# Optimization experiments

Hardware: AMD Instinct MI355X
Metric: run time of the kernel (lower is better)

Reference implementation:

```python
import jax, jax.numpy as jnp
import numpy as np

N_TP = 4  # number of heterogeneous agent types (experts)


def _mlp(x, w1, b1, w2, b2, w3, b3):
    h = jax.nn.relu(x @ w1 + b1)
    h = jax.nn.relu(h @ w2 + b2)
    return h @ w3 + b3


def setup_inputs() -> dict:
    key = jax.random.key(0)
    ks = jax.random.split(key, 12)
    T, A, D, H, NA = 2048, 128, 64, 64, 16
    s = 0.05
    return {
        "obs": jax.random.normal(ks[0], (T, A, D), dtype=jnp.float32),
        "hete_pick": jax.random.randint(ks[1], (T, A), 0, N_TP, dtype=jnp.int64),
        "gp_sel_summary": jax.random.uniform(ks[2], (T, N_TP), dtype=jnp.float32),
        "W1": jax.random.normal(ks[3], (N_TP, D + N_TP, H), dtype=jnp.float32) * s,
        "b1": jnp.zeros((N_TP, H), jnp.float32),
        "W2": jax.random.normal(ks[4], (N_TP, H, H), dtype=jnp.float32) * s,
        "b2": jnp.zeros((N_TP, H), jnp.float32),
        "W3": jax.random.normal(ks[5], (N_TP, H, NA), dtype=jnp.float32) * s,
        "b3": jnp.zeros((N_TP, NA), jnp.float32),
        "cW1": jax.random.normal(ks[6], (D + N_TP, H), dtype=jnp.float32) * s,
        "cb1": jnp.zeros((H,), jnp.float32),
        "cW2": jax.random.normal(ks[7], (H, H), dtype=jnp.float32) * s,
        "cb2": jnp.zeros((H,), jnp.float32),
        "cW3": jax.random.normal(ks[8], (H, 1), dtype=jnp.float32) * s,
        "cb3": jnp.zeros((1,), jnp.float32),
    }


def reference(obs, hete_pick, gp_sel_summary, W1, b1, W2, b2, W3, b3,
              cW1, cb1, cW2, cb2, cW3, cb3):
    T, A, D = obs.shape
    n_tp = W1.shape[0]
    # hete_info_obs: broadcast group-selection summary over agents, concat to obs
    hete_info = jnp.broadcast_to(gp_sel_summary[:, None, :], (T, A, n_tp))
    x = jnp.concatenate([obs, hete_info.astype(obs.dtype)], axis=-1)  # [T,A,D+n_tp]
    xf = x.reshape(T * A, D + n_tp)
    tp = hete_pick.reshape(T * A)
    # per-type dispatch: mask -> sub-net -> scatter back (expressed as masked select)
    logits = jnp.zeros((T * A, W3.shape[-1]), obs.dtype)
    for t in range(n_tp):
        out_t = _mlp(xf, W1[t], b1[t], W2[t], b2[t], W3[t], b3[t])
        logits = jnp.where((tp == t)[:, None], out_t, logits)
    # central critic runs on all agents
    value = _mlp(xf, cW1, cb1, cW2, cb2, cW3, cb3)  # [T*A,1]
    out = jnp.concatenate([logits, value], axis=-1)  # [T*A, n_action+1]
    return out.reshape(T, A, -1)
```

## Files before the change

kernel.cpp:

```cpp
#include <hip/hip_runtime.h>
#include <stdint.h>


typedef float v4f __attribute__((ext_vector_type(4)));
typedef short v8s __attribute__((ext_vector_type(8)));
typedef short v4s __attribute__((ext_vector_type(4)));
typedef float v4fa __attribute__((ext_vector_type(4), aligned(4)));

#define XS_STR 72
#define HS_STR 136
#define WP2_OFF  30720
#define WP3_OFF  51200
#define WPB2_OFF 56320

#define SEL4(te, a0, a1, a2, a3) \
    ((te) < 2 ? ((te) == 0 ? (a0) : (a1)) : ((te) == 2 ? (a2) : (a3)))

static __device__ __forceinline__ short f2bf(float f) {
    union { __bf16 b; short s; } u;
    u.b = (__bf16)f;
    return u.s;
}

static __device__ __forceinline__ v4s pack4r(const v4f a) {
    v4s r;
    r[0] = f2bf(fmaxf(a[0], 0.f));
    r[1] = f2bf(fmaxf(a[1], 0.f));
    r[2] = f2bf(fmaxf(a[2], 0.f));
    r[3] = f2bf(fmaxf(a[3], 0.f));
    return r;
}

__global__ void prep_kernel(const float* __restrict__ W1, const float* __restrict__ cW1,
                            const float* __restrict__ W2, const float* __restrict__ cW2,
                            const float* __restrict__ W3, const float* __restrict__ cW3,
                            const float* __restrict__ b1, const float* __restrict__ cb1,
                            const float* __restrict__ b2, const float* __restrict__ cb2,
                            short* __restrict__ wp) {
    int b = blockIdx.x, lane = threadIdx.x;
    int nl = lane & 15, quad = lane >> 4;
    short frag[8];
    if (b < 60) {
        int e = b / 12, rem = b % 12, ks = rem / 4, nt = rem % 4;
        int n = nt * 16 + nl;
#pragma unroll
        for (int j = 0; j < 8; j++) {
            int k = ks * 32 + quad * 8 + j;
            float v = 0.f;
            if (k < 68)       v = (e < 4) ? W1[(e * 68 + k) * 64 + n] : cW1[k * 64 + n];
            else if (k == 68) v = (e < 4) ? b1[e * 64 + n] : cb1[n];
            frag[j] = f2bf(v);
        }
    } else if (b < 100) {
        int u = b - 60, e = u / 8, ks = (u % 8) / 4, nt = u % 4;
        int n = nt * 16 + nl;
#pragma unroll
        for (int j = 0; j < 8; j++) {
            int k = ks * 32 + quad * 8 + j;
            frag[j] = f2bf((e < 4) ? W2[(e * 64 + k) * 64 + n] : cW2[k * 64 + n]);
        }
    } else if (b < 110) {
        int u = b - 100;
#pragma unroll
        for (int j = 0; j < 8; j++) {
            int ks = (u < 8) ? (u & 1) : (u - 8);
            int k  = ks * 32 + quad * 8 + j;
            float v;
            if (u < 8) { int ee = u >> 1; v = W3[(ee * 64 + k) * 16 + nl]; }
            else       { v = (nl == 0) ? cW3[k] : 0.f; }
            frag[j] = f2bf(v);
        }
    } else {
        int u = b - 110, net = u / 4, nt = u % 4;
        int n = nt * 16 + nl;
#pragma unroll
        for (int j = 0; j < 8; j++) {
            float v = 0.f;
            if (quad == 0 && j == 0) v = (net < 4) ? b2[net * 64 + n] : cb2[n];
            frag[j] = f2bf(v);
        }
    }
    v8s pk = { frag[0], frag[1], frag[2], frag[3], frag[4], frag[5], frag[6], frag[7] };
    *(v8s*)(wp + (size_t)b * 512 + lane * 8) = pk;
}


__global__ __launch_bounds__(256, 4) void main_kernel(
    const float* __restrict__ obs, const int* __restrict__ hete,
    const float* __restrict__ gp, const short* __restrict__ wp,
    const float* __restrict__ b3, const float* __restrict__ cb3,
    float* __restrict__ out)
{
    __shared__ __align__(16) short buf[128 * HS_STR];
    __shared__ int rowtok[128];
    __shared__ int tslot[128];
    __shared__ int wcnt[2][4];

    short* xs = buf;
    short* hs = buf;

    const int b = blockIdx.x;
    const int tid = threadIdx.x, lane = tid & 63, w = tid >> 6;
    const int ml = lane & 15, quad = lane >> 4;
    const size_t base = (size_t)b * 128;

    const int ltk = tid >> 1, hh = tid & 1;
    const float4* src = (const float4*)(obs + (base + ltk) * 64 + hh * 32);
    float4 f[8];
#pragma unroll
    for (int t = 0; t < 8; t++) f[t] = src[t];

    const float* gpb = gp + (size_t)b * 4;
    float g0 = gpb[0], g1 = gpb[1], g2 = gpb[2], g3 = gpb[3];

    int e = 0, rank = 0;
    if (tid < 128) {
        e = hete[base + tid];
        unsigned long long ltm = (1ull << lane) - 1ull;
        unsigned long long m0 = __ballot(e == 0);
        unsigned long long m1 = __ballot(e == 1);
        unsigned long long m2 = __ballot(e == 2);
        unsigned long long m3 = __ballot(e == 3);
        if      (e == 0) rank = __popcll(m0 & ltm);
        else if (e == 1) rank = __popcll(m1 & ltm);
        else if (e == 2) rank = __popcll(m2 & ltm);
        else             rank = __popcll(m3 & ltm);
        if (lane == 0) {
            wcnt[w][0] = __popcll(m0); wcnt[w][1] = __popcll(m1);
            wcnt[w][2] = __popcll(m2); wcnt[w][3] = __popcll(m3);
        }
    }
    __syncthreads();

    const int c0 = wcnt[0][0] + wcnt[1][0];
    const int c1 = wcnt[0][1] + wcnt[1][1];
    const int c2 = wcnt[0][2] + wcnt[1][2];
    const int sgs1 = __builtin_amdgcn_readfirstlane(c0);
    const int sgs2 = __builtin_amdgcn_readfirstlane(c0 + c1);
    const int sgs3 = __builtin_amdgcn_readfirstlane(c0 + c1 + c2);
    const int SG[5] = { 0, sgs1, sgs2, sgs3, 128 };

    if (tid < 128) {
        int gsE  = SEL4(e, 0, sgs1, sgs2, sgs3);
        int woff = (w == 1) ? wcnt[0][e] : 0;
        int slot = gsE + woff + rank;
        rowtok[slot] = tid;
        tslot[tid]   = slot;
    }
    __syncthreads();

    {
        int s  = tslot[ltk];
        int rb = s * XS_STR + hh * 32;
#pragma unroll
        for (int t = 0; t < 4; t++) {
            float4 a0 = f[2 * t], a1 = f[2 * t + 1];
            v8s pk = { f2bf(a0.x), f2bf(a0.y), f2bf(a0.z), f2bf(a0.w),
                       f2bf(a1.x), f2bf(a1.y), f2bf(a1.z), f2bf(a1.w) };
            *(v8s*)&xs[rb + t * 8] = pk;
        }
    }

    v8s gfrag = (v8s){0,0,0,0,0,0,0,0};
    v8s onef  = (v8s){0,0,0,0,0,0,0,0};
    if (quad == 0) {
        gfrag[0] = f2bf(g0); gfrag[1] = f2bf(g1);
        gfrag[2] = f2bf(g2); gfrag[3] = f2bf(g3);
        gfrag[4] = (short)0x3F80;
        onef[0]  = (short)0x3F80;
    }
    __syncthreads();

    v4f accE[8], accC[8], fx[3];
#pragma unroll
    for (int mt = 0; mt < 8; mt++) { accE[mt] = (v4f){0,0,0,0}; }
    fx[0] = fx[1] = fx[2] = (v4f){0,0,0,0};

    {
        v8s cW2 = *(const v8s*)(wp + (size_t)(14 * 4 + w) * 512 + lane * 8);
        v4f tC = __builtin_amdgcn_mfma_f32_16x16x32_bf16(cW2, gfrag, (v4f){0,0,0,0}, 0, 0, 0);
#pragma unroll
        for (int mt = 0; mt < 8; mt++) accC[mt] = tC;
    }
#pragma unroll
    for (int te = 0; te < 4; te++) {
        int lo = SG[te], hi = SG[te + 1];
        if (lo < hi) {
            v8s aW2 = *(const v8s*)(wp + (size_t)((te * 3 + 2) * 4 + w) * 512 + lane * 8);
            v4f tE = __builtin_amdgcn_mfma_f32_16x16x32_bf16(aW2, gfrag, (v4f){0,0,0,0}, 0, 0, 0);
#pragma unroll
            for (int mt = 0; mt < 8; mt++)
                if (mt * 16 >= lo && mt * 16 < hi) accE[mt] = tE;
            if (te > 0 && (lo & 15)) fx[te - 1] = tE;
        }
    }

    v8s cf1[2];
#pragma unroll
    for (int ks = 0; ks < 2; ks++)
        cf1[ks] = *(const v8s*)(wp + (size_t)((12 + ks) * 4 + w) * 512 + lane * 8);

#pragma unroll
    for (int ks = 0; ks < 2; ks++) {
#pragma unroll
        for (int mt = 0; mt < 8; mt++) {
            v8s xb = *(const v8s*)&xs[(mt * 16 + ml) * XS_STR + ks * 32 + quad * 8];
            accC[mt] = __builtin_amdgcn_mfma_f32_16x16x32_bf16(cf1[ks], xb, accC[mt], 0, 0, 0);
        }
#pragma unroll
        for (int te = 0; te < 4; te++) {
            int lo = SG[te], hi = SG[te + 1];
            if (lo < hi) {
                v8s aW = *(const v8s*)(wp + (size_t)((te * 3 + ks) * 4 + w) * 512 + lane * 8);
#pragma unroll
                for (int mt = 0; mt < 8; mt++) {
                    if (mt * 16 >= lo && mt * 16 < hi) {
                        v8s xb = *(const v8s*)&xs[(mt * 16 + ml) * XS_STR + ks * 32 + quad * 8];
                        accE[mt] = __builtin_amdgcn_mfma_f32_16x16x32_bf16(aW, xb, accE[mt], 0, 0, 0);
                    }
                    if (te > 0 && (lo & 15) && (lo >> 4) == mt) {
                        v8s xb = *(const v8s*)&xs[(mt * 16 + ml) * XS_STR + ks * 32 + quad * 8];
                        fx[te - 1] = __builtin_amdgcn_mfma_f32_16x16x32_bf16(aW, xb, fx[te - 1], 0, 0, 0);
                    }
                }
            }
        }
    }
    __syncthreads();

    {
#pragma unroll
        for (int mt = 0; mt < 8; mt++) {
            int rb = (mt * 16 + ml) * HS_STR + w * 16 + quad * 4;
            *(v4s*)&hs[rb]      = pack4r(accE[mt]);
            *(v4s*)&hs[rb + 64] = pack4r(accC[mt]);
        }
#pragma unroll
        for (int bb = 0; bb < 3; bb++) {
            int lo = SG[bb + 1], hi = SG[bb + 2];
            if ((lo & 15) && lo < hi) {
                int row  = (lo >> 4) * 16 + ml;
                int erow = (row >= sgs1) + (row >= sgs2) + (row >= sgs3);
                if (erow == bb + 1)
                    *(v4s*)&hs[row * HS_STR + w * 16 + quad * 4] = pack4r(fx[bb]);
            }
        }
    }
    __syncthreads();

    v4f acc2E[8], acc2C[8], fx2[3];
#pragma unroll
    for (int mt = 0; mt < 8; mt++) { acc2E[mt] = (v4f){0,0,0,0}; }
    fx2[0] = fx2[1] = fx2[2] = (v4f){0,0,0,0};

    {
        v8s cbf = *(const v8s*)(wp + WPB2_OFF + (size_t)(16 + w) * 512 + lane * 8);
        v4f tC = __builtin_amdgcn_mfma_f32_16x16x32_bf16(cbf, onef, (v4f){0,0,0,0}, 0, 0, 0);
#pragma unroll
        for (int mt = 0; mt < 8; mt++) acc2C[mt] = tC;
    }
#pragma unroll
    for (int te = 0; te < 4; te++) {
        int lo = SG[te], hi = SG[te + 1];
        if (lo < hi) {
            v8s bf = *(const v8s*)(wp + WPB2_OFF + (size_t)(te * 4 + w) * 512 + lane * 8);
            v4f tE = __builtin_amdgcn_mfma_f32_16x16x32_bf16(bf, onef, (v4f){0,0,0,0}, 0, 0, 0);
#pragma unroll
            for (int mt = 0; mt < 8; mt++)
                if (mt * 16 >= lo && mt * 16 < hi) acc2E[mt] = tE;
            if (te > 0 && (lo & 15)) fx2[te - 1] = tE;
        }
    }

    v8s cf2[2];
#pragma unroll
    for (int ks = 0; ks < 2; ks++)
        cf2[ks] = *(const v8s*)(wp + WP2_OFF + (size_t)((8 + ks) * 4 + w) * 512 + lane * 8);

#pragma unroll
    for (int ks = 0; ks < 2; ks++) {
#pragma unroll
        for (int mt = 0; mt < 8; mt++) {
            v8s hC = *(const v8s*)&hs[(mt * 16 + ml) * HS_STR + 64 + ks * 32 + quad * 8];
            acc2C[mt] = __builtin_amdgcn_mfma_f32_16x16x32_bf16(cf2[ks], hC, acc2C[mt], 0, 0, 0);
        }
#pragma unroll
        for (int te = 0; te < 4; te++) {
            int lo = SG[te], hi = SG[te + 1];
            if (lo < hi) {
                v8s aW = *(const v8s*)(wp + WP2_OFF + (size_t)((te * 2 + ks) * 4 + w) * 512 + lane * 8);
#pragma unroll
                for (int mt = 0; mt < 8; mt++) {
                    if (mt * 16 >= lo && mt * 16 < hi) {
                        v8s hE = *(const v8s*)&hs[(mt * 16 + ml) * HS_STR + ks * 32 + quad * 8];
                        acc2E[mt] = __builtin_amdgcn_mfma_f32_16x16x32_bf16(aW, hE, acc2E[mt], 0, 0, 0);
                    }
                    if (te > 0 && (lo & 15) && (lo >> 4) == mt) {
                        v8s hE = *(const v8s*)&hs[(mt * 16 + ml) * HS_STR + ks * 32 + quad * 8];
                        fx2[te - 1] = __builtin_amdgcn_mfma_f32_16x16x32_bf16(aW, hE, fx2[te - 1], 0, 0, 0);
                    }
                }
            }
        }
    }
    __syncthreads();

    {
#pragma unroll
        for (int mt = 0; mt < 8; mt++) {
            int rb = (mt * 16 + ml) * HS_STR + w * 16 + quad * 4;
            *(v4s*)&hs[rb]      = pack4r(acc2E[mt]);
            *(v4s*)&hs[rb + 64] = pack4r(acc2C[mt]);
        }
#pragma unroll
        for (int bb = 0; bb < 3; bb++) {
            int lo = SG[bb + 1], hi = SG[bb + 2];
            if ((lo & 15) && lo < hi) {
                int row  = (lo >> 4) * 16 + ml;
                int erow = (row >= sgs1) + (row >= sgs2) + (row >= sgs3);
                if (erow == bb + 1)
                    *(v4s*)&hs[row * HS_STR + w * 16 + quad * 4] = pack4r(fx2[bb]);
            }
        }
    }
    __syncthreads();

    v4f accL[2], accV[2];
#pragma unroll
    for (int j = 0; j < 2; j++) { accL[j] = (v4f){0,0,0,0}; accV[j] = (v4f){0,0,0,0}; }

#pragma unroll
    for (int ks = 0; ks < 2; ks++) {
        v8s aV = *(const v8s*)(wp + WP3_OFF + (size_t)(8 + ks) * 512 + lane * 8);
#pragma unroll
        for (int j = 0; j < 2; j++) {
            int mt = w + 4 * j;
            int te = (mt * 16 >= sgs1) + (mt * 16 >= sgs2) + (mt * 16 >= sgs3);
            v8s aW = *(const v8s*)(wp + WP3_OFF + (size_t)(te * 2 + ks) * 512 + lane * 8);
            v8s hE = *(const v8s*)&hs[(mt * 16 + ml) * HS_STR + ks * 32 + quad * 8];
            v8s hC = *(const v8s*)&hs[(mt * 16 + ml) * HS_STR + 64 + ks * 32 + quad * 8];
            accL[j] = __builtin_amdgcn_mfma_f32_16x16x32_bf16(aW, hE, accL[j], 0, 0, 0);
            accV[j] = __builtin_amdgcn_mfma_f32_16x16x32_bf16(aV, hC, accV[j], 0, 0, 0);
        }
    }

    v4f fxL[3];
#pragma unroll
    for (int bb = 0; bb < 3; bb++) {
        fxL[bb] = (v4f){0,0,0,0};
        int lo = SG[bb + 1], hi = SG[bb + 2];
        int mtb = lo >> 4;
        if ((lo & 15) && lo < hi && (mtb & 3) == w) {
#pragma unroll
            for (int ks = 0; ks < 2; ks++) {
                v8s aW = *(const v8s*)(wp + WP3_OFF + (size_t)((bb + 1) * 2 + ks) * 512 + lane * 8);
                v8s hE = *(const v8s*)&hs[(mtb * 16 + ml) * HS_STR + ks * 32 + quad * 8];
                fxL[bb] = __builtin_amdgcn_mfma_f32_16x16x32_bf16(aW, hE, fxL[bb], 0, 0, 0);
            }
        }
    }

    {
        float cb3v = cb3[0];
#pragma unroll
        for (int j = 0; j < 2; j++) {
            int mt = w + 4 * j;
            int te = (mt * 16 >= sgs1) + (mt * 16 >= sgs2) + (mt * 16 >= sgs3);
            int row = mt * 16 + ml;
            int erow = (row >= sgs1) + (row >= sgs2) + (row >= sgs3);
            int tk = rowtok[row];
            float* o = out + (base + (size_t)tk) * 17;
            if (erow == te) {
                v4fa b3v = *(const v4fa*)(b3 + te * 16 + quad * 4);
                v4fa ov = { accL[j][0] + b3v[0], accL[j][1] + b3v[1],
                            accL[j][2] + b3v[2], accL[j][3] + b3v[3] };
                *(v4fa*)(o + quad * 4) = ov;
            }
            if (quad == 0) o[16] = accV[j][0] + cb3v;
        }
#pragma unroll
        for (int bb = 0; bb < 3; bb++) {
            int lo = SG[bb + 1], hi = SG[bb + 2];
            int mtb = lo >> 4;
            if ((lo & 15) && lo < hi && (mtb & 3) == w) {
                int row = mtb * 16 + ml;
                int erow = (row >= sgs1) + (row >= sgs2) + (row >= sgs3);
                if (erow == bb + 1) {
                    v4fa b3v = *(const v4fa*)(b3 + (bb + 1) * 16 + quad * 4);
                    int tk = rowtok[row];
                    float* o = out + (base + (size_t)tk) * 17;
                    v4fa ov = { fxL[bb][0] + b3v[0], fxL[bb][1] + b3v[1],
                                fxL[bb][2] + b3v[2], fxL[bb][3] + b3v[3] };
                    *(v4fa*)(o + quad * 4) = ov;
                }
            }
        }
    }
}


extern "C" void kernel_launch(void* const* d_in, const int* in_sizes, int n_in,
                              void* d_out, int out_size, void* d_ws, size_t ws_size,
                              hipStream_t stream) {
    const float* obs = (const float*)d_in[0];
    const int*  hete = (const int*)d_in[1];
    const float* gp  = (const float*)d_in[2];
    const float* W1  = (const float*)d_in[3];
    const float* b1  = (const float*)d_in[4];
    const float* W2  = (const float*)d_in[5];
    const float* b2  = (const float*)d_in[6];
    const float* W3  = (const float*)d_in[7];
    const float* b3  = (const float*)d_in[8];
    const float* cW1 = (const float*)d_in[9];
    const float* cb1 = (const float*)d_in[10];
    const float* cW2 = (const float*)d_in[11];
    const float* cb2 = (const float*)d_in[12];
    const float* cW3 = (const float*)d_in[13];
    const float* cb3 = (const float*)d_in[14];
    float* out = (float*)d_out;

    short* wp = (short*)d_ws;

    prep_kernel<<<130,  64, 0, stream>>>(W1, cW1, W2, cW2, W3, cW3,
                                         b1, cb1, b2, cb2, wp);
    main_kernel<<<2048, 256, 0, stream>>>(obs, hete, gp, wp, b3, cb3, out);
}
```

Baseline: 159.4 us.

## Process two timesteps per block and prefetch next timestep's inputs during compute

Each block now handles two consecutive timesteps in a loop, halving the grid, and issues the global loads for the second timestep's obs, type ids and summary while the first timestep's layer-2 work runs. Tokens are no longer physically permuted into sorted slots in LDS; layer-1 reads gather rows through a per-lane rowtok index, which removes the tslot array. The goal is to hide global load latency and amortize per-block setup. The cost is higher register pressure from the prefetch buffers, which could lower occupancy, and fewer blocks to fill the GPU.

```diff
diff --git a/kernel.cpp b/kernel.cpp
--- a/kernel.cpp
+++ b/kernel.cpp
@@ -12,6 +12,7 @@
 #define WP2_OFF  30720
 #define WP3_OFF  51200
 #define WPB2_OFF 56320
+#define NT 2
 
 #define SEL4(te, a0, a1, a2, a3) \
     ((te) < 2 ? ((te) == 0 ? (a0) : (a1)) : ((te) == 2 ? (a2) : (a3)))
@@ -93,307 +94,330 @@
 {
     __shared__ __align__(16) short buf[128 * HS_STR];
     __shared__ int rowtok[128];
-    __shared__ int tslot[128];
     __shared__ int wcnt[2][4];
 
     short* xs = buf;
     short* hs = buf;
 
-    const int b = blockIdx.x;
     const int tid = threadIdx.x, lane = tid & 63, w = tid >> 6;
     const int ml = lane & 15, quad = lane >> 4;
-    const size_t base = (size_t)b * 128;
-
+    const int ts0 = blockIdx.x * NT;
     const int ltk = tid >> 1, hh = tid & 1;
-    const float4* src = (const float4*)(obs + (base + ltk) * 64 + hh * 32);
+
     float4 f[8];
-#pragma unroll
-    for (int t = 0; t < 8; t++) f[t] = src[t];
-
-    const float* gpb = gp + (size_t)b * 4;
-    float g0 = gpb[0], g1 = gpb[1], g2 = gpb[2], g3 = gpb[3];
-
-    int e = 0, rank = 0;
-    if (tid < 128) {
-        e = hete[base + tid];
-        unsigned long long ltm = (1ull << lane) - 1ull;
-        unsigned long long m0 = __ballot(e == 0);
-        unsigned long long m1 = __ballot(e == 1);
-        unsigned long long m2 = __ballot(e == 2);
-        unsigned long long m3 = __ballot(e == 3);
-        if      (e == 0) rank = __popcll(m0 & ltm);
-        else if (e == 1) rank = __popcll(m1 & ltm);
-        else if (e == 2) rank = __popcll(m2 & ltm);
-        else             rank = __popcll(m3 & ltm);
-        if (lane == 0) {
-            wcnt[w][0] = __popcll(m0); wcnt[w][1] = __popcll(m1);
-            wcnt[w][2] = __popcll(m2); wcnt[w][3] = __popcll(m3);
-        }
+    {
+        const float4* src = (const float4*)(obs + ((size_t)ts0 * 128 + ltk) * 64 + hh * 32);
+#pragma unroll
+        for (int t = 0; t < 8; t++) f[t] = src[t];
     }
-    __syncthreads();
-
-    const int c0 = wcnt[0][0] + wcnt[1][0];
-    const int c1 = wcnt[0][1] + wcnt[1][1];
-    const int c2 = wcnt[0][2] + wcnt[1][2];
-    const int sgs1 = __builtin_amdgcn_readfirstlane(c0);
-    const int sgs2 = __builtin_amdgcn_readfirstlane(c0 + c1);
-    const int sgs3 = __builtin_amdgcn_readfirstlane(c0 + c1 + c2);
-    const int SG[5] = { 0, sgs1, sgs2, sgs3, 128 };
-
-    if (tid < 128) {
-        int gsE  = SEL4(e, 0, sgs1, sgs2, sgs3);
-        int woff = (w == 1) ? wcnt[0][e] : 0;
-        int slot = gsE + woff + rank;
-        rowtok[slot] = tid;
-        tslot[tid]   = slot;
+    int ec = hete[(size_t)ts0 * 128 + (tid & 127)];
+    float g0, g1, g2, g3;
+    {
+        const float* gpb = gp + (size_t)ts0 * 4;
+        g0 = gpb[0]; g1 = gpb[1]; g2 = gpb[2]; g3 = gpb[3];
     }
-    __syncthreads();
-
-    {
-        int s  = tslot[ltk];
-        int rb = s * XS_STR + hh * 32;
-#pragma unroll
-        for (int t = 0; t < 4; t++) {
-            float4 a0 = f[2 * t], a1 = f[2 * t + 1];
-            v8s pk = { f2bf(a0.x), f2bf(a0.y), f2bf(a0.z), f2bf(a0.w),
-                       f2bf(a1.x), f2bf(a1.y), f2bf(a1.z), f2bf(a1.w) };
-            *(v8s*)&xs[rb + t * 8] = pk;
-        }
-    }
-
-    v8s gfrag = (v8s){0,0,0,0,0,0,0,0};
-    v8s onef  = (v8s){0,0,0,0,0,0,0,0};
-    if (quad == 0) {
-        gfrag[0] = f2bf(g0); gfrag[1] = f2bf(g1);
-        gfrag[2] = f2bf(g2); gfrag[3] = f2bf(g3);
-        gfrag[4] = (short)0x3F80;
-        onef[0]  = (short)0x3F80;
-    }
-    __syncthreads();
-
-    v4f accE[8], accC[8], fx[3];
-#pragma unroll
-    for (int mt = 0; mt < 8; mt++) { accE[mt] = (v4f){0,0,0,0}; }
-    fx[0] = fx[1] = fx[2] = (v4f){0,0,0,0};
-
-    {
-        v8s cW2 = *(const v8s*)(wp + (size_t)(14 * 4 + w) * 512 + lane * 8);
-        v4f tC = __builtin_amdgcn_mfma_f32_16x16x32_bf16(cW2, gfrag, (v4f){0,0,0,0}, 0, 0, 0);
-#pragma unroll
-        for (int mt = 0; mt < 8; mt++) accC[mt] = tC;
-    }
-#pragma unroll
-    for (int te = 0; te < 4; te++) {
-        int lo = SG[te], hi = SG[te + 1];
-        if (lo < hi) {
-            v8s aW2 = *(const v8s*)(wp + (size_t)((te * 3 + 2) * 4 + w) * 512 + lane * 8);
-            v4f tE = __builtin_amdgcn_mfma_f32_16x16x32_bf16(aW2, gfrag, (v4f){0,0,0,0}, 0, 0, 0);
-#pragma unroll
-            for (int mt = 0; mt < 8; mt++)
-                if (mt * 16 >= lo && mt * 16 < hi) accE[mt] = tE;
-            if (te > 0 && (lo & 15)) fx[te - 1] = tE;
-        }
-    }
-
-    v8s cf1[2];
-#pragma unroll
-    for (int ks = 0; ks < 2; ks++)
-        cf1[ks] = *(const v8s*)(wp + (size_t)((12 + ks) * 4 + w) * 512 + lane * 8);
-
-#pragma unroll
-    for (int ks = 0; ks < 2; ks++) {
-#pragma unroll
-        for (int mt = 0; mt < 8; mt++) {
-            v8s xb = *(const v8s*)&xs[(mt * 16 + ml) * XS_STR + ks * 32 + quad * 8];
-            accC[mt] = __builtin_amdgcn_mfma_f32_16x16x32_bf16(cf1[ks], xb, accC[mt], 0, 0, 0);
+    float4 fn[8];
+    int en = 0;
+    float n0 = 0.f, n1 = 0.f, n2 = 0.f, n3 = 0.f;
+
+    v8s onef = (v8s){0,0,0,0,0,0,0,0};
+    if (quad == 0) onef[0] = (short)0x3F80;
+
+#pragma unroll
+    for (int it = 0; it < NT; ++it) {
+        const size_t tbase = (size_t)(ts0 + it) * 128;
+        if (it) __syncthreads();
+
+        {
+            int rb = ltk * XS_STR + hh * 32;
+#pragma unroll
+            for (int t = 0; t < 4; t++) {
+                float4 a0 = f[2 * t], a1 = f[2 * t + 1];
+                v8s pk = { f2bf(a0.x), f2bf(a0.y), f2bf(a0.z), f2bf(a0.w),
+                           f2bf(a1.x), f2bf(a1.y), f2bf(a1.z), f2bf(a1.w) };
+                *(v8s*)&xs[rb + t * 8] = pk;
+            }
+        }
+
+        int e = ec, rank = 0;
+        if (tid < 128) {
+            unsigned long long ltm = (1ull << lane) - 1ull;
+            unsigned long long m0 = __ballot(e == 0);
+            unsigned long long m1 = __ballot(e == 1);
+            unsigned long long m2 = __ballot(e == 2);
+            unsigned long long m3 = __ballot(e == 3);
+            if      (e == 0) rank = __popcll(m0 & ltm);
+            else if (e == 1) rank = __popcll(m1 & ltm);
+            else if (e == 2) rank = __popcll(m2 & ltm);
+            else             rank = __popcll(m3 & ltm);
+            if (lane == 0) {
+                wcnt[w][0] = __popcll(m0); wcnt[w][1] = __popcll(m1);
+                wcnt[w][2] = __popcll(m2); wcnt[w][3] = __popcll(m3);
+            }
+        }
+        __syncthreads();
+
+        const int c0 = wcnt[0][0] + wcnt[1][0];
+        const int c1 = wcnt[0][1] + wcnt[1][1];
+        const int c2 = wcnt[0][2] + wcnt[1][2];
+        const int sgs1 = __builtin_amdgcn_readfirstlane(c0);
+        const int sgs2 = __builtin_amdgcn_readfirstlane(c0 + c1);
+        const int sgs3 = __builtin_amdgcn_readfirstlane(c0 + c1 + c2);
+        const int SG[5] = { 0, sgs1, sgs2, sgs3, 128 };
+
+        if (tid < 128) {
+            int gsE  = SEL4(e, 0, sgs1, sgs2, sgs3);
+            int woff = (w == 1) ? wcnt[0][e] : 0;
+            rowtok[gsE + woff + rank] = tid;
+        }
+        __syncthreads();
+
+        int tokR[8];
+#pragma unroll
+        for (int mt = 0; mt < 8; mt++) tokR[mt] = rowtok[mt * 16 + ml];
+
+        v8s gfrag = (v8s){0,0,0,0,0,0,0,0};
+        if (quad == 0) {
+            gfrag[0] = f2bf(g0); gfrag[1] = f2bf(g1);
+            gfrag[2] = f2bf(g2); gfrag[3] = f2bf(g3);
+            gfrag[4] = (short)0x3F80;
+        }
+
+        v4f accE[8], accC[8], fx[3];
+        fx[0] = fx[1] = fx[2] = (v4f){0,0,0,0};
+
+        {
+            v8s cWg = *(const v8s*)(wp + (size_t)(14 * 4 + w) * 512 + lane * 8);
+            v4f tC = __builtin_amdgcn_mfma_f32_16x16x32_bf16(cWg, gfrag, (v4f){0,0,0,0}, 0, 0, 0);
+#pragma unroll
+            for (int mt = 0; mt < 8; mt++) accC[mt] = tC;
         }
 #pragma unroll
         for (int te = 0; te < 4; te++) {
             int lo = SG[te], hi = SG[te + 1];
             if (lo < hi) {
-                v8s aW = *(const v8s*)(wp + (size_t)((te * 3 + ks) * 4 + w) * 512 + lane * 8);
-#pragma unroll
-                for (int mt = 0; mt < 8; mt++) {
-                    if (mt * 16 >= lo && mt * 16 < hi) {
-                        v8s xb = *(const v8s*)&xs[(mt * 16 + ml) * XS_STR + ks * 32 + quad * 8];
-                        accE[mt] = __builtin_amdgcn_mfma_f32_16x16x32_bf16(aW, xb, accE[mt], 0, 0, 0);
+                v8s aW2 = *(const v8s*)(wp + (size_t)((te * 3 + 2) * 4 + w) * 512 + lane * 8);
+                v4f tE = __builtin_amdgcn_mfma_f32_16x16x32_bf16(aW2, gfrag, (v4f){0,0,0,0}, 0, 0, 0);
+#pragma unroll
+                for (int mt = 0; mt < 8; mt++)
+                    if (mt * 16 >= lo && mt * 16 < hi) accE[mt] = tE;
+                if (te > 0 && (lo & 15)) fx[te - 1] = tE;
+            }
+        }
+
+        v8s cf1[2];
+#pragma unroll
+        for (int ks = 0; ks < 2; ks++)
+            cf1[ks] = *(const v8s*)(wp + (size_t)((12 + ks) * 4 + w) * 512 + lane * 8);
+
+#pragma unroll
+        for (int ks = 0; ks < 2; ks++) {
+#pragma unroll
+            for (int mt = 0; mt < 8; mt++) {
+                v8s xb = *(const v8s*)&xs[tokR[mt] * XS_STR + ks * 32 + quad * 8];
+                accC[mt] = __builtin_amdgcn_mfma_f32_16x16x32_bf16(cf1[ks], xb, accC[mt], 0, 0, 0);
+            }
+#pragma unroll
+            for (int te = 0; te < 4; te++) {
+                int lo = SG[te], hi = SG[te + 1];
+                if (lo < hi) {
+                    v8s aW = *(const v8s*)(wp + (size_t)((te * 3 + ks) * 4 + w) * 512 + lane * 8);
+#pragma unroll
+                    for (int mt = 0; mt < 8; mt++) {
+                        if (mt * 16 >= lo && mt * 16 < hi) {
+                            v8s xb = *(const v8s*)&xs[tokR[mt] * XS_STR + ks * 32 + quad * 8];
+                            accE[mt] = __builtin_amdgcn_mfma_f32_16x16x32_bf16(aW, xb, accE[mt], 0, 0, 0);
+                        }
+                        if (te > 0 && (lo & 15) && (lo >> 4) == mt) {
+                            v8s xb = *(const v8s*)&xs[tokR[mt] * XS_STR + ks * 32 + quad * 8];
+                            fx[te - 1] = __builtin_amdgcn_mfma_f32_16x16x32_bf16(aW, xb, fx[te - 1], 0, 0, 0);
+                        }
                     }
-                    if (te > 0 && (lo & 15) && (lo >> 4) == mt) {
-                        v8s xb = *(const v8s*)&xs[(mt * 16 + ml) * XS_STR + ks * 32 + quad * 8];
-                        fx[te - 1] = __builtin_amdgcn_mfma_f32_16x16x32_bf16(aW, xb, fx[te - 1], 0, 0, 0);
-                    }
-                }
-            }
-        }
-    }
-    __syncthreads();
-
-    {
-#pragma unroll
-        for (int mt = 0; mt < 8; mt++) {
-            int rb = (mt * 16 + ml) * HS_STR + w * 16 + quad * 4;
-            *(v4s*)&hs[rb]      = pack4r(accE[mt]);
-            *(v4s*)&hs[rb + 64] = pack4r(accC[mt]);
-        }
-#pragma unroll
-        for (int bb = 0; bb < 3; bb++) {
-            int lo = SG[bb + 1], hi = SG[bb + 2];
-            if ((lo & 15) && lo < hi) {
-                int row  = (lo >> 4) * 16 + ml;
-                int erow = (row >= sgs1) + (row >= sgs2) + (row >= sgs3);
-                if (erow == bb + 1)
-                    *(v4s*)&hs[row * HS_STR + w * 16 + quad * 4] = pack4r(fx[bb]);
-            }
-        }
-    }
-    __syncthreads();
-
-    v4f acc2E[8], acc2C[8], fx2[3];
-#pragma unroll
-    for (int mt = 0; mt < 8; mt++) { acc2E[mt] = (v4f){0,0,0,0}; }
-    fx2[0] = fx2[1] = fx2[2] = (v4f){0,0,0,0};
-
-    {
-        v8s cbf = *(const v8s*)(wp + WPB2_OFF + (size_t)(16 + w) * 512 + lane * 8);
-        v4f tC = __builtin_amdgcn_mfma_f32_16x16x32_bf16(cbf, onef, (v4f){0,0,0,0}, 0, 0, 0);
-#pragma unroll
-        for (int mt = 0; mt < 8; mt++) acc2C[mt] = tC;
-    }
-#pragma unroll
-    for (int te = 0; te < 4; te++) {
-        int lo = SG[te], hi = SG[te + 1];
-        if (lo < hi) {
-            v8s bf = *(const v8s*)(wp + WPB2_OFF + (size_t)(te * 4 + w) * 512 + lane * 8);
-            v4f tE = __builtin_amdgcn_mfma_f32_16x16x32_bf16(bf, onef, (v4f){0,0,0,0}, 0, 0, 0);
-#pragma unroll
-            for (int mt = 0; mt < 8; mt++)
-                if (mt * 16 >= lo && mt * 16 < hi) acc2E[mt] = tE;
-            if (te > 0 && (lo & 15)) fx2[te - 1] = tE;
-        }
-    }
-
-    v8s cf2[2];
-#pragma unroll
-    for (int ks = 0; ks < 2; ks++)
-        cf2[ks] = *(const v8s*)(wp + WP2_OFF + (size_t)((8 + ks) * 4 + w) * 512 + lane * 8);
-
-#pragma unroll
-    for (int ks = 0; ks < 2; ks++) {
-#pragma unroll
-        for (int mt = 0; mt < 8; mt++) {
-            v8s hC = *(const v8s*)&hs[(mt * 16 + ml) * HS_STR + 64 + ks * 32 + quad * 8];
-            acc2C[mt] = __builtin_amdgcn_mfma_f32_16x16x32_bf16(cf2[ks], hC, acc2C[mt], 0, 0, 0);
+                }
+            }
+        }
+        __syncthreads();
+
+        if (it == 0) {
+            const float4* srcn = (const float4*)(obs + ((size_t)(ts0 + 1) * 128 + ltk) * 64 + hh * 32);
+#pragma unroll
+            for (int t = 0; t < 8; t++) fn[t] = srcn[t];
+            en = hete[(size_t)(ts0 + 1) * 128 + (tid & 127)];
+            const float* gpn = gp + (size_t)(ts0 + 1) * 4;
+            n0 = gpn[0]; n1 = gpn[1]; n2 = gpn[2]; n3 = gpn[3];
+        }
+
+        {
+#pragma unroll
+            for (int mt = 0; mt < 8; mt++) {
+                int rb = (mt * 16 + ml) * HS_STR + w * 16 + quad * 4;
+                *(v4s*)&hs[rb]      = pack4r(accE[mt]);
+                *(v4s*)&hs[rb + 64] = pack4r(accC[mt]);
+            }
+#pragma unroll
+            for (int bb = 0; bb < 3; bb++) {
+                int lo = SG[bb + 1], hi = SG[bb + 2];
+                if ((lo & 15) && lo < hi) {
+                    int row  = (lo >> 4) * 16 + ml;
+                    int erow = (row >= sgs1) + (row >= sgs2) + (row >= sgs3);
+                    if (erow == bb + 1)
+                        *(v4s*)&hs[row * HS_STR + w * 16 + quad * 4] = pack4r(fx[bb]);
+                }
+            }
+        }
+        __syncthreads();
+
+        v4f acc2E[8], acc2C[8], fx2[3];
+        fx2[0] = fx2[1] = fx2[2] = (v4f){0,0,0,0};
+
+        {
+            v8s cbf = *(const v8s*)(wp + WPB2_OFF + (size_t)(16 + w) * 512 + lane * 8);
+            v4f tC = __builtin_amdgcn_mfma_f32_16x16x32_bf16(cbf, onef, (v4f){0,0,0,0}, 0, 0, 0);
+#pragma unroll
+            for (int mt = 0; mt < 8; mt++) acc2C[mt] = tC;
         }
 #pragma unroll
         for (int te = 0; te < 4; te++) {
             int lo = SG[te], hi = SG[te + 1];
             if (lo < hi) {
-                v8s aW = *(const v8s*)(wp + WP2_OFF + (size_t)((te * 2 + ks) * 4 + w) * 512 + lane * 8);
-#pragma unroll
-                for (int mt = 0; mt < 8; mt++) {
-                    if (mt * 16 >= lo && mt * 16 < hi) {
-                        v8s hE = *(const v8s*)&hs[(mt * 16 + ml) * HS_STR + ks * 32 + quad * 8];
-                        acc2E[mt] = __builtin_amdgcn_mfma_f32_16x16x32_bf16(aW, hE, acc2E[mt], 0, 0, 0);
+                v8s bf = *(const v8s*)(wp + WPB2_OFF + (size_t)(te * 4 + w) * 512 + lane * 8);
+                v4f tE = __builtin_amdgcn_mfma_f32_16x16x32_bf16(bf, onef, (v4f){0,0,0,0}, 0, 0, 0);
+#pragma unroll
+                for (int mt = 0; mt < 8; mt++)
+                    if (mt * 16 >= lo && mt * 16 < hi) acc2E[mt] = tE;
+                if (te > 0 && (lo & 15)) fx2[te - 1] = tE;
+            }
+        }
+
+        v8s cf2[2];
+#pragma unroll
+        for (int ks = 0; ks < 2; ks++)
+            cf2[ks] = *(const v8s*)(wp + WP2_OFF + (size_t)((8 + ks) * 4 + w) * 512 + lane * 8);
+
+#pragma unroll
+        for (int ks = 0; ks < 2; ks++) {
+#pragma unroll
+            for (int mt = 0; mt < 8; mt++) {
+                v8s hC = *(const v8s*)&hs[(mt * 16 + ml) * HS_STR + 64 + ks * 32 + quad * 8];
+                acc2C[mt] = __builtin_amdgcn_mfma_f32_16x16x32_bf16(cf2[ks], hC, acc2C[mt], 0, 0, 0);
+            }
+#pragma unroll
+            for (int te = 0; te < 4; te++) {
+                int lo = SG[te], hi = SG[te + 1];
+                if (lo < hi) {
+                    v8s aW = *(const v8s*)(wp + WP2_OFF + (size_t)((te * 2 + ks) * 4 + w) * 512 + lane * 8);
+#pragma unroll
+                    for (int mt = 0; mt < 8; mt++) {
+                        if (mt * 16 >= lo && mt * 16 < hi) {
+                            v8s hE = *(const v8s*)&hs[(mt * 16 + ml) * HS_STR + ks * 32 + quad * 8];
+                            acc2E[mt] = __builtin_amdgcn_mfma_f32_16x16x32_bf16(aW, hE, acc2E[mt], 0, 0, 0);
+                        }
+                        if (te > 0 && (lo & 15) && (lo >> 4) == mt) {
+                            v8s hE = *(const v8s*)&hs[(mt * 16 + ml) * HS_STR + ks * 32 + quad * 8];
+                            fx2[te - 1] = __builtin_amdgcn_mfma_f32_16x16x32_bf16(aW, hE, fx2[te - 1], 0, 0, 0);
+                        }
                     }
-                    if (te > 0 && (lo & 15) && (lo >> 4) == mt) {
-                        v8s hE = *(const v8s*)&hs[(mt * 16 + ml) * HS_STR + ks * 32 + quad * 8];
-                        fx2[te - 1] = __builtin_amdgcn_mfma_f32_16x16x32_bf16(aW, hE, fx2[te - 1], 0, 0, 0);
-                    }
-                }
-            }
-        }
-    }
-    __syncthreads();
-
-    {
-#pragma unroll
-        for (int mt = 0; mt < 8; mt++) {
-            int rb = (mt * 16 + ml) * HS_STR + w * 16 + quad * 4;
-            *(v4s*)&hs[rb]      = pack4r(acc2E[mt]);
-            *(v4s*)&hs[rb + 64] = pack4r(acc2C[mt]);
-        }
+                }
+            }
+        }
+        __syncthreads();
+
+        {
+#pragma unroll
+            for (int mt = 0; mt < 8; mt++) {
+                int rb = (mt * 16 + ml) * HS_STR + w * 16 + quad * 4;
+                *(v4s*)&hs[rb]      = pack4r(acc2E[mt]);
+                *(v4s*)&hs[rb + 64] = pack4r(acc2C[mt]);
+            }
+#pragma unroll
+            for (int bb = 0; bb < 3; bb++) {
+                int lo = SG[bb + 1], hi = SG[bb + 2];
+                if ((lo & 15) && lo < hi) {
+                    int row  = (lo >> 4) * 16 + ml;
+                    int erow = (row >= sgs1) + (row >= sgs2) + (row >= sgs3);
+                    if (erow == bb + 1)
+                        *(v4s*)&hs[row * HS_STR + w * 16 + quad * 4] = pack4r(fx2[bb]);
+                }
+            }
+        }
+        __syncthreads();
+
+        v4f accL[2], accV[2];
+#pragma unroll
+        for (int j = 0; j < 2; j++) { accL[j] = (v4f){0,0,0,0}; accV[j] = (v4f){0,0,0,0}; }
+
+#pragma unroll
+        for (int ks = 0; ks < 2; ks++) {
+            v8s aV = *(const v8s*)(wp + WP3_OFF + (size_t)(8 + ks) * 512 + lane * 8);
+#pragma unroll
+            for (int j = 0; j < 2; j++) {
+                int mt = w + 4 * j;
+                int te = (mt * 16 >= sgs1) + (mt * 16 >= sgs2) + (mt * 16 >= sgs3);
+                v8s aW = *(const v8s*)(wp + WP3_OFF + (size_t)(te * 2 + ks) * 512 + lane * 8);
+                v8s hE = *(const v8s*)&hs[(mt * 16 + ml) * HS_STR + ks * 32 + quad * 8];
+                v8s hC = *(const v8s*)&hs[(mt * 16 + ml) * HS_STR + 64 + ks * 32 + quad * 8];
+                accL[j] = __builtin_amdgcn_mfma_f32_16x16x32_bf16(aW, hE, accL[j], 0, 0, 0);
+                accV[j] = __builtin_amdgcn_mfma_f32_16x16x32_bf16(aV, hC, accV[j], 0, 0, 0);
+            }
+        }
+
+        v4f fxL[3];
 #pragma unroll
         for (int bb = 0; bb < 3; bb++) {
-            int lo = SG[bb + 1], hi = SG[bb + 2];
-            if ((lo & 15) && lo < hi) {
-                int row  = (lo >> 4) * 16 + ml;
-                int erow = (row >= sgs1) + (row >= sgs2) + (row >= sgs3);
-                if (erow == bb + 1)
-                    *(v4s*)&hs[row * HS_STR + w * 16 + quad * 4] = pack4r(fx2[bb]);
-            }
-        }
-    }
-    __syncthreads();
-
-    v4f accL[2], accV[2];
-#pragma unroll
-    for (int j = 0; j < 2; j++) { accL[j] = (v4f){0,0,0,0}; accV[j] = (v4f){0,0,0,0}; }
-
-#pragma unroll
-    for (int ks = 0; ks < 2; ks++) {
-        v8s aV = *(const v8s*)(wp + WP3_OFF + (size_t)(8 + ks) * 512 + lane * 8);
-#pragma unroll
-        for (int j = 0; j < 2; j++) {
-            int mt = w + 4 * j;
-            int te = (mt * 16 >= sgs1) + (mt * 16 >= sgs2) + (mt * 16 >= sgs3);
-            v8s aW = *(const v8s*)(wp + WP3_OFF + (size_t)(te * 2 + ks) * 512 + lane * 8);
-            v8s hE = *(const v8s*)&hs[(mt * 16 + ml) * HS_STR + ks * 32 + quad * 8];
-            v8s hC = *(const v8s*)&hs[(mt * 16 + ml) * HS_STR + 64 + ks * 32 + quad * 8];
-            accL[j] = __builtin_amdgcn_mfma_f32_16x16x32_bf16(aW, hE, accL[j], 0, 0, 0);
-            accV[j] = __builtin_amdgcn_mfma_f32_16x16x32_bf16(aV, hC, accV[j], 0, 0, 0);
-        }
-    }
-
-    v4f fxL[3];
-#pragma unroll
-    for (int bb = 0; bb < 3; bb++) {
-        fxL[bb] = (v4f){0,0,0,0};
-        int lo = SG[bb + 1], hi = SG[bb + 2];
-        int mtb = lo >> 4;
-        if ((lo & 15) && lo < hi && (mtb & 3) == w) {
-#pragma unroll
-            for (int ks = 0; ks < 2; ks++) {
-                v8s aW = *(const v8s*)(wp + WP3_OFF + (size_t)((bb + 1) * 2 + ks) * 512 + lane * 8);
-                v8s hE = *(const v8s*)&hs[(mtb * 16 + ml) * HS_STR + ks * 32 + quad * 8];
-                fxL[bb] = __builtin_amdgcn_mfma_f32_16x16x32_bf16(aW, hE, fxL[bb], 0, 0, 0);
-            }
-        }
-    }
-
-    {
-        float cb3v = cb3[0];
-#pragma unroll
-        for (int j = 0; j < 2; j++) {
-            int mt = w + 4 * j;
-            int te = (mt * 16 >= sgs1) + (mt * 16 >= sgs2) + (mt * 16 >= sgs3);
-            int row = mt * 16 + ml;
-            int erow = (row >= sgs1) + (row >= sgs2) + (row >= sgs3);
-            int tk = rowtok[row];
-            float* o = out + (base + (size_t)tk) * 17;
-            if (erow == te) {
-                v4fa b3v = *(const v4fa*)(b3 + te * 16 + quad * 4);
-                v4fa ov = { accL[j][0] + b3v[0], accL[j][1] + b3v[1],
-                            accL[j][2] + b3v[2], accL[j][3] + b3v[3] };
-                *(v4fa*)(o + quad * 4) = ov;
-            }
-            if (quad == 0) o[16] = accV[j][0] + cb3v;
-        }
-#pragma unroll
-        for (int bb = 0; bb < 3; bb++) {
+            fxL[bb] = (v4f){0,0,0,0};
             int lo = SG[bb + 1], hi = SG[bb + 2];
             int mtb = lo >> 4;
             if ((lo & 15) && lo < hi && (mtb & 3) == w) {
-                int row = mtb * 16 + ml;
+#pragma unroll
+                for (int ks = 0; ks < 2; ks++) {
+                    v8s aW = *(const v8s*)(wp + WP3_OFF + (size_t)((bb + 1) * 2 + ks) * 512 + lane * 8);
+                    v8s hE = *(const v8s*)&hs[(mtb * 16 + ml) * HS_STR + ks * 32 + quad * 8];
+                    fxL[bb] = __builtin_amdgcn_mfma_f32_16x16x32_bf16(aW, hE, fxL[bb], 0, 0, 0);
+                }
+            }
+        }
+
+        {
+            float cb3v = cb3[0];
+#pragma unroll
+            for (int j = 0; j < 2; j++) {
+                int mt = w + 4 * j;
+                int te = (mt * 16 >= sgs1) + (mt * 16 >= sgs2) + (mt * 16 >= sgs3);
+                int row = mt * 16 + ml;
                 int erow = (row >= sgs1) + (row >= sgs2) + (row >= sgs3);
-                if (erow == bb + 1) {
-                    v4fa b3v = *(const v4fa*)(b3 + (bb + 1) * 16 + quad * 4);
-                    int tk = rowtok[row];
-                    float* o = out + (base + (size_t)tk) * 17;
-                    v4fa ov = { fxL[bb][0] + b3v[0], fxL[bb][1] + b3v[1],
-                                fxL[bb][2] + b3v[2], fxL[bb][3] + b3v[3] };
+                int tk = rowtok[row];
+                float* o = out + (tbase + (size_t)tk) * 17;
+                if (erow == te) {
+                    v4fa b3v = *(const v4fa*)(b3 + te * 16 + quad * 4);
+                    v4fa ov = { accL[j][0] + b3v[0], accL[j][1] + b3v[1],
+                                accL[j][2] + b3v[2], accL[j][3] + b3v[3] };
                     *(v4fa*)(o + quad * 4) = ov;
                 }
-            }
+                if (quad == 0) o[16] = accV[j][0] + cb3v;
+            }
+#pragma unroll
+            for (int bb = 0; bb < 3; bb++) {
+                int lo = SG[bb + 1], hi = SG[bb + 2];
+                int mtb = lo >> 4;
+                if ((lo & 15) && lo < hi && (mtb & 3) == w) {
+                    int row = mtb * 16 + ml;
+                    int erow = (row >= sgs1) + (row >= sgs2) + (row >= sgs3);
+                    if (erow == bb + 1) {
+                        v4fa b3v = *(const v4fa*)(b3 + (bb + 1) * 16 + quad * 4);
+                        int tk = rowtok[row];
+                        float* o = out + (tbase + (size_t)tk) * 17;
+                        v4fa ov = { fxL[bb][0] + b3v[0], fxL[bb][1] + b3v[1],
+                                    fxL[bb][2] + b3v[2], fxL[bb][3] + b3v[3] };
+                        *(v4fa*)(o + quad * 4) = ov;
+                    }
+                }
+            }
+        }
+
+        if (it == 0) {
+#pragma unroll
+            for (int t = 0; t < 8; t++) f[t] = fn[t];
+            ec = en; g0 = n0; g1 = n1; g2 = n2; g3 = n3;
         }
     }
 }
@@ -423,5 +447,5 @@
 
     prep_kernel<<<130,  64, 0, stream>>>(W1, cW1, W2, cW2, W3, cW3,
                                          b1, cb1, b2, cb2, wp);
-    main_kernel<<<2048, 256, 0, stream>>>(obs, hete, gp, wp, b3, cb3, out);
+    main_kernel<<<1024, 256, 0, stream>>>(obs, hete, gp, wp, b3, cb3, out);
 }
```

Result: slower. 223.8 us (+40.4%).
